# Optimization experiments

Measured on AMD Instinct MI355X. Metric: run time of the kernel, lower is better.

Reference implementation:

```python
import jax, jax.numpy as jnp
import numpy as np

N = 100000      # number of edge features (rows of feats)
M = 800000      # number of triplets
HID = 128
HEADS = 8
DH = HID // HEADS


def setup_inputs() -> dict:
    key = jax.random.key(0)
    ks = jax.random.split(key, 10)
    s = 1.0 / np.sqrt(HID)
    inp = {
        "feats": jax.random.normal(ks[0], (N, HID), dtype=jnp.float32),
        "idx_kj": jax.random.randint(ks[1], (M,), 0, N, dtype=jnp.int64),
        "idx_ji": jax.random.randint(ks[2], (M,), 0, N, dtype=jnp.int64),
        "Wv": jax.random.uniform(ks[3], (HID, HID), jnp.float32, -s, s),
        "Wq": jax.random.uniform(ks[4], (HID, HID), jnp.float32, -s, s),
        "Wk": jax.random.uniform(ks[5], (HID, HID), jnp.float32, -s, s),
        "W1": jax.random.uniform(ks[6], (HID, HID), jnp.float32, -s, s),
        "b1": jax.random.uniform(ks[7], (HID,), jnp.float32, -s, s),
        "W2": jax.random.uniform(ks[8], (HID, HID), jnp.float32, -s, s),
        "b2": jax.random.uniform(ks[9], (HID,), jnp.float32, -s, s),
    }
    return inp


def reference(feats, idx_kj, idx_ji, Wv, Wq, Wk, W1, b1, W2, b2):
    # Projections (no bias), reshape to [N, H, Dh]
    v = (feats @ Wv.T).reshape(N, HEADS, DH)
    k = (feats @ Wk.T).reshape(N, HEADS, DH)
    q = (feats @ Wq.T).reshape(N, HEADS, DH)

    # edge-indexed attention scores: [M, H, 1]
    att = jnp.sum(q[idx_kj] * k[idx_ji], axis=-1, keepdims=True)
    att = jnp.exp(jax.nn.leaky_relu(att, negative_slope=0.2))  # unsafe softmax, as in source

    # segment-sum normalizer over destination index idx_ji: [N, H, 1]
    denom = jax.ops.segment_sum(att, idx_ji, num_segments=N)
    att = att / denom[idx_ji]

    # weighted V gather-scatter: [M, HID] -> [N, HID]
    v_att = (v[idx_kj] * att).reshape(M, HID)
    agg = jax.ops.segment_sum(v_att, idx_ji, num_segments=N)  # v_clone after +scatter-v

    v_flat = v.reshape(N, HID)
    # ResidualLayer (dropout in eval mode -> identity): v + relu(lin2(relu(lin1(agg))))
    h = jax.nn.relu(agg @ W1.T + b1)
    h = jax.nn.relu(h @ W2.T + b2)
    return v_flat + h
```

## Files before the change

kernel.cpp:

```cpp
#include <hip/hip_runtime.h>
#include <hip/hip_bf16.h>
#include <math.h>

#define N_NODES 100000
#define M_EDGES 800000
#define HID 128
#define HEADS 8
#define DH 16
#define SCAN_NB ((N_NODES + 1023) / 1024)

typedef __attribute__((ext_vector_type(8))) short short8;
typedef __attribute__((ext_vector_type(4))) float floatx4;

__device__ __forceinline__ ushort f32_to_bf16(float x) {
    __hip_bfloat16 h = __float2bfloat16(x);
    union { __hip_bfloat16 h; ushort u; } c; c.h = h;
    return c.u;
}
__device__ __forceinline__ float bf16_bits_to_f32(ushort u) {
    union { unsigned int i; float f; } c; c.i = ((unsigned int)u) << 16;
    return c.f;
}
__device__ __forceinline__ float bf16pair_lo(unsigned int p) {
    union { unsigned int i; float f; } c; c.i = p << 16; return c.f;
}
__device__ __forceinline__ float bf16pair_hi(unsigned int p) {
    union { unsigned int i; float f; } c; c.i = p & 0xffff0000u; return c.f;
}

__global__ __launch_bounds__(256) void cvt_w_kernel(
    const float* __restrict__ Wq, const float* __restrict__ Wk, const float* __restrict__ Wv,
    const float* __restrict__ W1, const float* __restrict__ W2,
    ushort* __restrict__ dq, ushort* __restrict__ dk, ushort* __restrict__ dv,
    ushort* __restrict__ d1, ushort* __restrict__ d2,
    int* __restrict__ count)
{
    int i = blockIdx.x * 256 + threadIdx.x;
    if (i < 5 * 16384) {
        int w = i >> 14;
        int o = i & 16383;
        int j    = o & 7;
        int lane = (o >> 3) & 63;
        int f    = o >> 9;
        int t    = f & 7, ks = f >> 3;
        int row  = t * 16 + (lane & 15);
        int col  = ks * 32 + (lane >> 4) * 8 + j;
        const float* s[5] = {Wq, Wk, Wv, W1, W2};
        ushort*      d[5] = {dq, dk, dv, d1, d2};
        d[w][o] = f32_to_bf16(s[w][row * HID + col]);
    }
    if (i < N_NODES) count[i] = 0;
}

__device__ __forceinline__ void stage_w_lin(const ushort* __restrict__ Wf,
                                            ushort* __restrict__ lds, int tid)
{
    #pragma unroll
    for (int i = 0; i < 8; ++i) {
        int idx = (i * 256 + tid) * 8;
        *(uint4*)(lds + idx) = *(const uint4*)(Wf + idx);
    }
}

__global__ __launch_bounds__(256) void qkv_mfma_kernel(
    const float* __restrict__ feats,
    const ushort* __restrict__ Wq16, const ushort* __restrict__ Wk16, const ushort* __restrict__ Wv16,
    ushort* __restrict__ qv16, ushort* __restrict__ k16)
{
    __shared__ ushort wlds[16384];
    const int tid  = threadIdx.x;
    const int wave = tid >> 6;
    const int lane = tid & 63;
    const int row0 = blockIdx.x * 128 + wave * 32;
    const int lrow = lane & 15;
    const int lk   = (lane >> 4) * 8;
    const int crow = (lane >> 4) * 4;

    short8 afrag[2][4];
    bool tvalid[2];
    #pragma unroll
    for (int r = 0; r < 2; ++r) {
        int rr = row0 + r * 16;
        tvalid[r] = (rr < N_NODES);
        const float* arow = feats + (size_t)((tvalid[r] ? rr : 0) + lrow) * HID + lk;
        #pragma unroll
        for (int ks = 0; ks < 4; ++ks) {
            float4 f0 = *(const float4*)(arow + ks * 32);
            float4 f1 = *(const float4*)(arow + ks * 32 + 4);
            short8 a;
            a[0] = (short)f32_to_bf16(f0.x); a[1] = (short)f32_to_bf16(f0.y);
            a[2] = (short)f32_to_bf16(f0.z); a[3] = (short)f32_to_bf16(f0.w);
            a[4] = (short)f32_to_bf16(f1.x); a[5] = (short)f32_to_bf16(f1.y);
            a[6] = (short)f32_to_bf16(f1.z); a[7] = (short)f32_to_bf16(f1.w);
            afrag[r][ks] = a;
        }
    }

    const ushort* Ws[3] = {Wq16, Wk16, Wv16};
    ushort* Ob[3]; int Ostride[3];
    Ob[0] = qv16;       Ostride[0] = 256;
    Ob[1] = k16;        Ostride[1] = 128;
    Ob[2] = qv16 + 128; Ostride[2] = 256;

    #pragma unroll
    for (int w = 0; w < 3; ++w) {
        __syncthreads();
        stage_w_lin(Ws[w], wlds, tid);
        __syncthreads();

        floatx4 acc[2][8];
        #pragma unroll
        for (int r = 0; r < 2; ++r)
            #pragma unroll
            for (int t = 0; t < 8; ++t) acc[r][t] = (floatx4)(0.f);

        #pragma unroll
        for (int ks = 0; ks < 4; ++ks) {
            short8 B[8];
            #pragma unroll
            for (int t = 0; t < 8; ++t)
                B[t] = *(const short8*)&wlds[(ks * 8 + t) * 512 + lane * 8];
            #pragma unroll
            for (int t = 0; t < 8; ++t) {
                acc[0][t] = __builtin_amdgcn_mfma_f32_16x16x32_bf16(B[t], afrag[0][ks], acc[0][t], 0, 0, 0);
                acc[1][t] = __builtin_amdgcn_mfma_f32_16x16x32_bf16(B[t], afrag[1][ks], acc[1][t], 0, 0, 0);
            }
        }

        #pragma unroll
        for (int r = 0; r < 2; ++r) {
            if (tvalid[r]) {
                ushort* O = Ob[w] + (size_t)(row0 + r * 16 + lrow) * Ostride[w];
                #pragma unroll
                for (int t = 0; t < 8; ++t) {
                    ushort4 o;
                    o.x = f32_to_bf16(acc[r][t][0]); o.y = f32_to_bf16(acc[r][t][1]);
                    o.z = f32_to_bf16(acc[r][t][2]); o.w = f32_to_bf16(acc[r][t][3]);
                    *(ushort4*)(O + t * 16 + crow) = o;
                }
            }
        }
    }
}

__global__ __launch_bounds__(256) void hist_kernel(
    const int* __restrict__ idx_ji, int* __restrict__ count)
{
    int m = blockIdx.x * 256 + threadIdx.x;
    if (m < M_EDGES) atomicAdd(&count[idx_ji[m]], 1);
}

__global__ __launch_bounds__(256) void scan_blocksum_kernel(
    const int* __restrict__ count, int* __restrict__ blocksum)
{
    __shared__ int s[256];
    const int tid = threadIdx.x;
    const int base = blockIdx.x * 1024 + tid * 4;
    int sum = 0;
    if (base + 3 < N_NODES) {
        int4 c = *(const int4*)(count + base);
        sum = c.x + c.y + c.z + c.w;
    } else {
        #pragma unroll
        for (int j = 0; j < 4; ++j) if (base + j < N_NODES) sum += count[base + j];
    }
    s[tid] = sum;
    __syncthreads();
    for (int off = 128; off > 0; off >>= 1) {
        if (tid < off) s[tid] += s[tid + off];
        __syncthreads();
    }
    if (tid == 0) blocksum[blockIdx.x] = s[0];
}

__global__ __launch_bounds__(256) void scan_write_kernel(
    const int* __restrict__ count, const int* __restrict__ blocksum,
    int* __restrict__ offsets, int* __restrict__ cursor)
{
    __shared__ int s[256];
    __shared__ int sb[256];
    const int tid = threadIdx.x;
    const int base = blockIdx.x * 1024 + tid * 4;

    sb[tid] = (tid < (int)blockIdx.x && tid < SCAN_NB) ? blocksum[tid] : 0;
    __syncthreads();
    for (int off = 128; off > 0; off >>= 1) {
        if (tid < off) sb[tid] += sb[tid + off];
        __syncthreads();
    }
    const int bbase = sb[0];

    int c0 = 0, c1 = 0, c2 = 0, c3 = 0;
    if (base + 3 < N_NODES) {
        int4 c = *(const int4*)(count + base);
        c0 = c.x; c1 = c.y; c2 = c.z; c3 = c.w;
    } else {
        if (base     < N_NODES) c0 = count[base];
        if (base + 1 < N_NODES) c1 = count[base + 1];
        if (base + 2 < N_NODES) c2 = count[base + 2];
        if (base + 3 < N_NODES) c3 = count[base + 3];
    }
    const int tsum = c0 + c1 + c2 + c3;
    s[tid] = tsum;
    __syncthreads();
    for (int off = 1; off < 256; off <<= 1) {
        int x = (tid >= off) ? s[tid - off] : 0;
        __syncthreads();
        s[tid] += x;
        __syncthreads();
    }
    int o0 = s[tid] - tsum + bbase;
    int o1 = o0 + c0, o2 = o1 + c1, o3 = o2 + c2;
    if (base + 3 < N_NODES) {
        *(int4*)(offsets + base) = make_int4(o0, o1, o2, o3);
        *(int4*)(cursor  + base) = make_int4(o0, o1, o2, o3);
    } else {
        if (base     < N_NODES) { offsets[base]     = o0; cursor[base]     = o0; }
        if (base + 1 < N_NODES) { offsets[base + 1] = o1; cursor[base + 1] = o1; }
        if (base + 2 < N_NODES) { offsets[base + 2] = o2; cursor[base + 2] = o2; }
        if (base + 3 < N_NODES) { offsets[base + 3] = o3; cursor[base + 3] = o3; }
    }
}

__global__ __launch_bounds__(256) void fill_kernel(
    const int* __restrict__ idx_ji, const int* __restrict__ idx_kj,
    int* __restrict__ cursor, int* __restrict__ edge_kj)
{
    int m = blockIdx.x * 256 + threadIdx.x;
    if (m < M_EDGES) {
        int pos = atomicAdd(&cursor[idx_ji[m]], 1);
        edge_kj[pos] = idx_kj[m];
    }
}

__device__ __forceinline__ float dot8(const uint4& qp, const float* kn) {
    const unsigned int* q = (const unsigned int*)&qp;
    float p = 0.f;
    #pragma unroll
    for (int j = 0; j < 4; ++j)
        p += bf16pair_lo(q[j]) * kn[2*j] + bf16pair_hi(q[j]) * kn[2*j+1];
    return p;
}
__device__ __forceinline__ void axpy8(float* acc, float s, const uint4& vp) {
    const unsigned int* v = (const unsigned int*)&vp;
    #pragma unroll
    for (int j = 0; j < 4; ++j) {
        acc[2*j]   += s * bf16pair_lo(v[j]);
        acc[2*j+1] += s * bf16pair_hi(v[j]);
    }
}

__global__ __launch_bounds__(256) void aggregate_kernel(
    const int* __restrict__ edge_kj, const int* __restrict__ offsets,
    const int* __restrict__ count, const ushort* __restrict__ qv16,
    const ushort* __restrict__ k16, ushort* __restrict__ agg16)
{
    const int gid  = blockIdx.x * 256 + threadIdx.x;
    const int node = gid >> 4;
    const int l16  = threadIdx.x & 15;
    if (node >= N_NODES) return;

    const int deg  = count[node];
    const int base = offsets[node];

    float kn[8];
    {
        uint4 kp = *(const uint4*)(k16 + (size_t)node * HID + l16 * 8);
        const unsigned int* kw = (const unsigned int*)&kp;
        #pragma unroll
        for (int j = 0; j < 4; ++j) {
            kn[2*j]   = bf16pair_lo(kw[j]);
            kn[2*j+1] = bf16pair_hi(kw[j]);
        }
    }

    float acc[8] = {0.f,0.f,0.f,0.f,0.f,0.f,0.f,0.f};
    float d = 0.f;

    const ushort* qvb = qv16 + l16 * 8;

    int e = 0;
    for (; e + 4 <= deg; e += 4) {
        const int kj0 = edge_kj[base + e + 0];
        const int kj1 = edge_kj[base + e + 1];
        const int kj2 = edge_kj[base + e + 2];
        const int kj3 = edge_kj[base + e + 3];
        const ushort* r0 = qvb + (size_t)kj0 * 256;
        const ushort* r1 = qvb + (size_t)kj1 * 256;
        const ushort* r2 = qvb + (size_t)kj2 * 256;
        const ushort* r3 = qvb + (size_t)kj3 * 256;
        uint4 qp0 = *(const uint4*)r0;  uint4 vp0 = *(const uint4*)(r0 + 128);
        uint4 qp1 = *(const uint4*)r1;  uint4 vp1 = *(const uint4*)(r1 + 128);
        uint4 qp2 = *(const uint4*)r2;  uint4 vp2 = *(const uint4*)(r2 + 128);
        uint4 qp3 = *(const uint4*)r3;  uint4 vp3 = *(const uint4*)(r3 + 128);

        float p0 = dot8(qp0, kn);
        float p1 = dot8(qp1, kn);
        float p2 = dot8(qp2, kn);
        float p3 = dot8(qp3, kn);
        p0 += __shfl_xor(p0, 1);
        p1 += __shfl_xor(p1, 1);
        p2 += __shfl_xor(p2, 1);
        p3 += __shfl_xor(p3, 1);
        float s0 = __expf(fmaxf(p0, 0.2f * p0));
        float s1 = __expf(fmaxf(p1, 0.2f * p1));
        float s2 = __expf(fmaxf(p2, 0.2f * p2));
        float s3 = __expf(fmaxf(p3, 0.2f * p3));
        d += (s0 + s1) + (s2 + s3);
        axpy8(acc, s0, vp0);
        axpy8(acc, s1, vp1);
        axpy8(acc, s2, vp2);
        axpy8(acc, s3, vp3);
    }
    if (e + 2 <= deg) {
        const int kj0 = edge_kj[base + e];
        const int kj1 = edge_kj[base + e + 1];
        const ushort* r0 = qvb + (size_t)kj0 * 256;
        const ushort* r1 = qvb + (size_t)kj1 * 256;
        uint4 qp0 = *(const uint4*)r0;  uint4 vp0 = *(const uint4*)(r0 + 128);
        uint4 qp1 = *(const uint4*)r1;  uint4 vp1 = *(const uint4*)(r1 + 128);
        float p0 = dot8(qp0, kn);
        float p1 = dot8(qp1, kn);
        p0 += __shfl_xor(p0, 1);
        p1 += __shfl_xor(p1, 1);
        float s0 = __expf(fmaxf(p0, 0.2f * p0));
        float s1 = __expf(fmaxf(p1, 0.2f * p1));
        d += s0 + s1;
        axpy8(acc, s0, vp0);
        axpy8(acc, s1, vp1);
        e += 2;
    }
    if (e < deg) {
        const int kj0 = edge_kj[base + e];
        const ushort* r0 = qvb + (size_t)kj0 * 256;
        uint4 qp0 = *(const uint4*)r0;  uint4 vp0 = *(const uint4*)(r0 + 128);
        float p0 = dot8(qp0, kn);
        p0 += __shfl_xor(p0, 1);
        float s0 = __expf(fmaxf(p0, 0.2f * p0));
        d += s0;
        axpy8(acc, s0, vp0);
    }

    const float inv = (deg > 0) ? 1.f / d : 0.f;
    uint4 o;
    unsigned int* ow = (unsigned int*)&o;
    #pragma unroll
    for (int j = 0; j < 4; ++j)
        ow[j] = (unsigned int)f32_to_bf16(acc[2*j] * inv)
              | ((unsigned int)f32_to_bf16(acc[2*j+1] * inv) << 16);
    *(uint4*)(agg16 + (size_t)node * HID + l16 * 8) = o;
}

__global__ __launch_bounds__(256) void mlp_mfma_kernel(
    const ushort* __restrict__ agg16, const ushort* __restrict__ qv16,
    const ushort* __restrict__ W1f, const float* __restrict__ b1,
    const ushort* __restrict__ W2f, const float* __restrict__ b2,
    float* __restrict__ out)
{
    __shared__ ushort wlds[16384];
    __shared__ ushort hs[4][16 * 136];
    const int tid  = threadIdx.x;
    const int wave = tid >> 6;
    const int lane = tid & 63;
    const int row0 = blockIdx.x * 128 + wave * 32;
    const int lrow = lane & 15;
    const int lk   = (lane >> 4) * 8;
    const int crow = (lane >> 4) * 4;

    short8 afrag[2][4];
    bool tvalid[2];
    #pragma unroll
    for (int r = 0; r < 2; ++r) {
        int rr = row0 + r * 16;
        tvalid[r] = (rr < N_NODES);
        const ushort* arow = agg16 + (size_t)((tvalid[r] ? rr : 0) + lrow) * HID + lk;
        #pragma unroll
        for (int ks = 0; ks < 4; ++ks)
            afrag[r][ks] = *(const short8*)(arow + ks * 32);
    }

    stage_w_lin(W1f, wlds, tid);
    __syncthreads();

    short8 hfrag[2][4];
    ushort* sc = &hs[wave][0];
    #pragma unroll
    for (int r = 0; r < 2; ++r) {
        floatx4 acc[8];
        #pragma unroll
        for (int t = 0; t < 8; ++t) acc[t] = (floatx4)(0.f);
        #pragma unroll
        for (int ks = 0; ks < 4; ++ks) {
            short8 B[8];
            #pragma unroll
            for (int t = 0; t < 8; ++t)
                B[t] = *(const short8*)&wlds[(ks * 8 + t) * 512 + lane * 8];
            #pragma unroll
            for (int t = 0; t < 8; ++t)
                acc[t] = __builtin_amdgcn_mfma_f32_16x16x32_bf16(B[t], afrag[r][ks], acc[t], 0, 0, 0);
        }
        #pragma unroll
        for (int t = 0; t < 8; ++t) {
            float4 bias = *(const float4*)(b1 + t * 16 + crow);
            ushort4 o;
            o.x = f32_to_bf16(fmaxf(acc[t][0] + bias.x, 0.f));
            o.y = f32_to_bf16(fmaxf(acc[t][1] + bias.y, 0.f));
            o.z = f32_to_bf16(fmaxf(acc[t][2] + bias.z, 0.f));
            o.w = f32_to_bf16(fmaxf(acc[t][3] + bias.w, 0.f));
            *(ushort4*)(sc + lrow * 136 + t * 16 + crow) = o;
        }
        #pragma unroll
        for (int ks = 0; ks < 4; ++ks)
            hfrag[r][ks] = *(const short8*)(sc + lrow * 136 + ks * 32 + lk);
    }
    __syncthreads();
    stage_w_lin(W2f, wlds, tid);
    __syncthreads();

    {
        floatx4 acc[2][8];
        #pragma unroll
        for (int r = 0; r < 2; ++r)
            #pragma unroll
            for (int t = 0; t < 8; ++t) acc[r][t] = (floatx4)(0.f);
        #pragma unroll
        for (int ks = 0; ks < 4; ++ks) {
            short8 B[8];
            #pragma unroll
            for (int t = 0; t < 8; ++t)
                B[t] = *(const short8*)&wlds[(ks * 8 + t) * 512 + lane * 8];
            #pragma unroll
            for (int t = 0; t < 8; ++t) {
                acc[0][t] = __builtin_amdgcn_mfma_f32_16x16x32_bf16(B[t], hfrag[0][ks], acc[0][t], 0, 0, 0);
                acc[1][t] = __builtin_amdgcn_mfma_f32_16x16x32_bf16(B[t], hfrag[1][ks], acc[1][t], 0, 0, 0);
            }
        }
        #pragma unroll
        for (int r = 0; r < 2; ++r) {
            if (tvalid[r]) {
                const size_t nrow = (size_t)(row0 + r * 16 + lrow);
                const ushort* vrow = qv16 + nrow * 256 + 128;
                float* orow = out + nrow * HID;
                #pragma unroll
                for (int t = 0; t < 8; ++t) {
                    float4 bias = *(const float4*)(b2 + t * 16 + crow);
                    ushort4 vv = *(const ushort4*)(vrow + t * 16 + crow);
                    float4 o;
                    o.x = bf16_bits_to_f32(vv.x) + fmaxf(acc[r][t][0] + bias.x, 0.f);
                    o.y = bf16_bits_to_f32(vv.y) + fmaxf(acc[r][t][1] + bias.y, 0.f);
                    o.z = bf16_bits_to_f32(vv.z) + fmaxf(acc[r][t][2] + bias.z, 0.f);
                    o.w = bf16_bits_to_f32(vv.w) + fmaxf(acc[r][t][3] + bias.w, 0.f);
                    *(float4*)(orow + t * 16 + crow) = o;
                }
            }
        }
    }
}

extern "C" void kernel_launch(void* const* d_in, const int* in_sizes, int n_in,
                              void* d_out, int out_size, void* d_ws, size_t ws_size,
                              hipStream_t stream) {
    const float* feats  = (const float*)d_in[0];
    const int*   idx_kj = (const int*)d_in[1];
    const int*   idx_ji = (const int*)d_in[2];
    const float* Wv     = (const float*)d_in[3];
    const float* Wq     = (const float*)d_in[4];
    const float* Wk     = (const float*)d_in[5];
    const float* W1     = (const float*)d_in[6];
    const float* b1     = (const float*)d_in[7];
    const float* W2     = (const float*)d_in[8];
    const float* b2     = (const float*)d_in[9];
    float* out = (float*)d_out;

    ushort* qv16    = (ushort*)d_ws;
    ushort* k16     = qv16    + (size_t)N_NODES * 256;
    ushort* agg16   = k16     + (size_t)N_NODES * HID;
    ushort* Wq16    = agg16   + (size_t)N_NODES * HID;
    ushort* Wk16    = Wq16 + HID * HID;
    ushort* Wv16    = Wk16 + HID * HID;
    ushort* W116    = Wv16 + HID * HID;
    ushort* W216    = W116 + HID * HID;
    int* count      = (int*)(W216 + HID * HID);
    int* offsets    = count + N_NODES;
    int* cursor     = offsets + N_NODES;
    int* blocksum   = cursor + N_NODES;
    int* edge_kj    = blocksum + ((SCAN_NB + 3) & ~3);

    cvt_w_kernel<<<(N_NODES + 255) / 256, 256, 0, stream>>>(
        Wq, Wk, Wv, W1, W2, Wq16, Wk16, Wv16, W116, W216, count);

    qkv_mfma_kernel<<<(N_NODES + 127) / 128, 256, 0, stream>>>(
        feats, Wq16, Wk16, Wv16, qv16, k16);

    hist_kernel<<<(M_EDGES + 255) / 256, 256, 0, stream>>>(idx_ji, count);
    scan_blocksum_kernel<<<SCAN_NB, 256, 0, stream>>>(count, blocksum);
    scan_write_kernel<<<SCAN_NB, 256, 0, stream>>>(count, blocksum, offsets, cursor);
    fill_kernel<<<(M_EDGES + 255) / 256, 256, 0, stream>>>(idx_ji, idx_kj, cursor, edge_kj);

    aggregate_kernel<<<((size_t)N_NODES * 16 + 255) / 256, 256, 0, stream>>>(
        edge_kj, offsets, count, qv16, k16, agg16);

    mlp_mfma_kernel<<<(N_NODES + 127) / 128, 256, 0, stream>>>(
        agg16, qv16, W116, b1, W216, b2, out);
}
```

Before: 322.8 us.

## Split QKV projection per weight across blocks and fuse histogram into same launch

Each QKV block now computes only one of the three projections (chosen by block index) instead of looping over all three, which triples the grid and shortens each block. The weight staging no longer needs repeated barriers. The edge histogram atomics are appended as extra blocks in the same launch, so the histogram overlaps with the projection GEMMs and one kernel launch is removed. In exchange, each feats row tile is loaded and converted to bf16 three times.

```diff
diff --git a/kernel.cpp b/kernel.cpp
--- a/kernel.cpp
+++ b/kernel.cpp
@@ -8,6 +8,9 @@
 #define HEADS 8
 #define DH 16
 #define SCAN_NB ((N_NODES + 1023) / 1024)
+#define NRT 782
+#define NQKV (3 * NRT)
+#define NHIST ((M_EDGES + 255) / 256)
 
 typedef __attribute__((ext_vector_type(8))) short short8;
 typedef __attribute__((ext_vector_type(4))) float floatx4;
@@ -62,19 +65,35 @@
     }
 }
 
-__global__ __launch_bounds__(256) void qkv_mfma_kernel(
+__global__ __launch_bounds__(256) void qkv_hist_kernel(
     const float* __restrict__ feats,
     const ushort* __restrict__ Wq16, const ushort* __restrict__ Wk16, const ushort* __restrict__ Wv16,
-    ushort* __restrict__ qv16, ushort* __restrict__ k16)
+    ushort* __restrict__ qv16, ushort* __restrict__ k16,
+    const int* __restrict__ idx_ji, int* __restrict__ count)
 {
     __shared__ ushort wlds[16384];
     const int tid  = threadIdx.x;
+
+    if (blockIdx.x >= NQKV) {
+        int m = (blockIdx.x - NQKV) * 256 + tid;
+        if (m < M_EDGES) atomicAdd(&count[idx_ji[m]], 1);
+        return;
+    }
+
+    const int w    = blockIdx.x / NRT;
+    const int rt   = blockIdx.x % NRT;
     const int wave = tid >> 6;
     const int lane = tid & 63;
-    const int row0 = blockIdx.x * 128 + wave * 32;
+    const int row0 = rt * 128 + wave * 32;
     const int lrow = lane & 15;
     const int lk   = (lane >> 4) * 8;
     const int crow = (lane >> 4) * 4;
+
+    const ushort* Wf = (w == 0) ? Wq16 : (w == 1) ? Wk16 : Wv16;
+    ushort* Ob       = (w == 0) ? qv16 : (w == 1) ? k16  : qv16 + 128;
+    const int Ostr   = (w == 1) ? 128 : 256;
+
+    stage_w_lin(Wf, wlds, tid);
 
     short8 afrag[2][4];
     bool tvalid[2];
@@ -96,58 +115,40 @@
         }
     }
 
-    const ushort* Ws[3] = {Wq16, Wk16, Wv16};
-    ushort* Ob[3]; int Ostride[3];
-    Ob[0] = qv16;       Ostride[0] = 256;
-    Ob[1] = k16;        Ostride[1] = 128;
-    Ob[2] = qv16 + 128; Ostride[2] = 256;
-
-    #pragma unroll
-    for (int w = 0; w < 3; ++w) {
-        __syncthreads();
-        stage_w_lin(Ws[w], wlds, tid);
-        __syncthreads();
-
-        floatx4 acc[2][8];
-        #pragma unroll
-        for (int r = 0; r < 2; ++r)
-            #pragma unroll
-            for (int t = 0; t < 8; ++t) acc[r][t] = (floatx4)(0.f);
-
-        #pragma unroll
-        for (int ks = 0; ks < 4; ++ks) {
-            short8 B[8];
-            #pragma unroll
-            for (int t = 0; t < 8; ++t)
-                B[t] = *(const short8*)&wlds[(ks * 8 + t) * 512 + lane * 8];
+    __syncthreads();
+
+    floatx4 acc[2][8];
+    #pragma unroll
+    for (int r = 0; r < 2; ++r)
+        #pragma unroll
+        for (int t = 0; t < 8; ++t) acc[r][t] = (floatx4)(0.f);
+
+    #pragma unroll
+    for (int ks = 0; ks < 4; ++ks) {
+        short8 B[8];
+        #pragma unroll
+        for (int t = 0; t < 8; ++t)
+            B[t] = *(const short8*)&wlds[(ks * 8 + t) * 512 + lane * 8];
+        #pragma unroll
+        for (int t = 0; t < 8; ++t) {
+            acc[0][t] = __builtin_amdgcn_mfma_f32_16x16x32_bf16(B[t], afrag[0][ks], acc[0][t], 0, 0, 0);
+            acc[1][t] = __builtin_amdgcn_mfma_f32_16x16x32_bf16(B[t], afrag[1][ks], acc[1][t], 0, 0, 0);
+        }
+    }
+
+    #pragma unroll
+    for (int r = 0; r < 2; ++r) {
+        if (tvalid[r]) {
+            ushort* O = Ob + (size_t)(row0 + r * 16 + lrow) * Ostr;
             #pragma unroll
             for (int t = 0; t < 8; ++t) {
-                acc[0][t] = __builtin_amdgcn_mfma_f32_16x16x32_bf16(B[t], afrag[0][ks], acc[0][t], 0, 0, 0);
-                acc[1][t] = __builtin_amdgcn_mfma_f32_16x16x32_bf16(B[t], afrag[1][ks], acc[1][t], 0, 0, 0);
+                ushort4 o;
+                o.x = f32_to_bf16(acc[r][t][0]); o.y = f32_to_bf16(acc[r][t][1]);
+                o.z = f32_to_bf16(acc[r][t][2]); o.w = f32_to_bf16(acc[r][t][3]);
+                *(ushort4*)(O + t * 16 + crow) = o;
             }
         }
-
-        #pragma unroll
-        for (int r = 0; r < 2; ++r) {
-            if (tvalid[r]) {
-                ushort* O = Ob[w] + (size_t)(row0 + r * 16 + lrow) * Ostride[w];
-                #pragma unroll
-                for (int t = 0; t < 8; ++t) {
-                    ushort4 o;
-                    o.x = f32_to_bf16(acc[r][t][0]); o.y = f32_to_bf16(acc[r][t][1]);
-                    o.z = f32_to_bf16(acc[r][t][2]); o.w = f32_to_bf16(acc[r][t][3]);
-                    *(ushort4*)(O + t * 16 + crow) = o;
-                }
-            }
-        }
-    }
-}
-
-__global__ __launch_bounds__(256) void hist_kernel(
-    const int* __restrict__ idx_ji, int* __restrict__ count)
-{
-    int m = blockIdx.x * 256 + threadIdx.x;
-    if (m < M_EDGES) atomicAdd(&count[idx_ji[m]], 1);
+    }
 }
 
 __global__ __launch_bounds__(256) void scan_blocksum_kernel(
@@ -489,10 +490,9 @@
     cvt_w_kernel<<<(N_NODES + 255) / 256, 256, 0, stream>>>(
         Wq, Wk, Wv, W1, W2, Wq16, Wk16, Wv16, W116, W216, count);
 
-    qkv_mfma_kernel<<<(N_NODES + 127) / 128, 256, 0, stream>>>(
-        feats, Wq16, Wk16, Wv16, qv16, k16);
-
-    hist_kernel<<<(M_EDGES + 255) / 256, 256, 0, stream>>>(idx_ji, count);
+    qkv_hist_kernel<<<NQKV + NHIST, 256, 0, stream>>>(
+        feats, Wq16, Wk16, Wv16, qv16, k16, idx_ji, count);
+
     scan_blocksum_kernel<<<SCAN_NB, 256, 0, stream>>>(count, blocksum);
     scan_write_kernel<<<SCAN_NB, 256, 0, stream>>>(count, blocksum, offsets, cursor);
     fill_kernel<<<(M_EDGES + 255) / 256, 256, 0, stream>>>(idx_ji, idx_kj, cursor, edge_kj);
```

Result: no change. 319.3 us (median of 2 runs) (-1.1%).
